# Kernel tuning notes

Hardware: AMD Instinct MI355X
Metric: run time of the kernel (lower is better)

The kernel has to match this reference:

```python
import jax, jax.numpy as jnp
import numpy as np

IN_DIM = 256
QK_DIM = IN_DIM // 8


def setup_inputs() -> dict:
    key = jax.random.key(0)
    ks = jax.random.split(key, 10)
    B, C, W, H = 4, IN_DIM, 64, 64
    a = jax.random.normal(ks[0], (B, C, W, H), dtype=jnp.float32)
    b = jax.random.normal(ks[1], (B, C, W, H), dtype=jnp.float32)
    c = jax.random.uniform(ks[2], (B, 1, 2 * W, 2 * H), dtype=jnp.float32)
    scale = 0.02
    wq = jax.random.normal(ks[3], (QK_DIM, C), dtype=jnp.float32) * scale
    bq = jnp.zeros((QK_DIM,), dtype=jnp.float32)
    wk = jax.random.normal(ks[4], (QK_DIM, C), dtype=jnp.float32) * scale
    bk = jnp.zeros((QK_DIM,), dtype=jnp.float32)
    wv = jax.random.normal(ks[5], (C, C), dtype=jnp.float32) * scale
    bv = jnp.zeros((C,), dtype=jnp.float32)
    gamma = jnp.ones((1,), dtype=jnp.float32)
    return {"a": a, "b": b, "c": c, "wq": wq, "bq": bq, "wk": wk,
            "bk": bk, "wv": wv, "bv": bv, "gamma": gamma}


def reference(a, b, c, wq, bq, wk, bk, wv, bv, gamma):
    B, C, W, H = a.shape
    N = W * H
    # F.interpolate(c, scale_factor=1/down_rate, mode='nearest'): output idx i -> input idx i*down_rate
    down = c.shape[2] // W
    cd = c[:, :, ::down, ::down]                      # [B,1,W,H]
    # 1x1 convs as channel contractions
    q = jnp.einsum('bchw,oc->bohw', a, wq) + bq[None, :, None, None]
    k = jnp.einsum('bchw,oc->bohw', b, wk) + bk[None, :, None, None]
    v = jnp.einsum('bchw,oc->bohw', a, wv) + bv[None, :, None, None]
    qf = q.reshape(B, QK_DIM, N)                      # proj_query^T rows are spatial
    kf = k.reshape(B, QK_DIM, N)
    vf = v.reshape(B, C, N)
    sim = jnp.einsum('bdi,bdj->bij', qf, kf)          # [B,N,N]
    cflat = cd.reshape(B, N)
    # mask[b,i,j] = cflat[b,i] (per-query multiplicative logit scaling)
    logits = sim * cflat[:, :, None]
    attn = jax.nn.softmax(logits, axis=-1)            # [B,N,N]
    out_attn = jnp.einsum('bcj,bij->bci', vf, attn).reshape(B, C, W, H)
    out = gamma * a * cd + (1.0 - cd) * out_attn
    return out
```

## Files before the change

kernel.cpp:

```cpp
#include <hip/hip_runtime.h>

#define LOG2E 1.44269504088896340736f

typedef __attribute__((ext_vector_type(8))) short short8;
typedef __attribute__((ext_vector_type(4))) float float4v;
typedef __attribute__((ext_vector_type(2))) float float2v;
typedef __attribute__((ext_vector_type(2))) int int2v;
typedef __attribute__((ext_vector_type(4))) int int4v;

__device__ inline unsigned short f2bf(float f) {
    union { float f; unsigned u; } v; v.f = f;
    unsigned r = v.u + 0x7fffu + ((v.u >> 16) & 1u);
    return (unsigned short)(r >> 16);
}
__device__ inline float bf2f(unsigned short u) {
    union { unsigned u; float f; } v; v.u = ((unsigned)u) << 16;
    return v.f;
}
__device__ inline unsigned pk_bf16(float a, float b) {
    union { float f; unsigned u; } ua, ub; ua.f = a; ub.f = b;
    return __builtin_amdgcn_perm(ub.u + 0x8000u, ua.u + 0x8000u, 0x07060302u);
}
__device__ inline unsigned cvtpk_bf16(float a, float b) {
    unsigned r;
    asm("v_cvt_pk_bf16_f32 %0, %1, %2" : "=v"(r) : "v"(a), "v"(b));
    return r;
}

__global__ void wcvt_kernel(const float* __restrict__ wq, const float* __restrict__ wk,
                            const float* __restrict__ wv, unsigned short* __restrict__ Wbf)
{
    int idx = blockIdx.x * 256 + threadIdx.x;
    int e4  = idx * 4;
    int row = e4 >> 8, col = e4 & 255;
    const float* src = (row < 32) ? (wq + row * 256 + col)
                     : (row < 64) ? (wk + (row - 32) * 256 + col)
                                  : (wv + (row - 64) * 256 + col);
    float4v v = *(const float4v*)src;
    int2v p;
    p.x = (unsigned)f2bf(v[0]) | ((unsigned)f2bf(v[1]) << 16);
    p.y = (unsigned)f2bf(v[2]) | ((unsigned)f2bf(v[3]) << 16);
    *(int2v*)(Wbf + e4) = p;
}

__launch_bounds__(512, 2)
__global__ void proj_kernel(const float* __restrict__ a_p, const float* __restrict__ b_p,
                            const float* __restrict__ c_p,
                            const float* __restrict__ bq, const float* __restrict__ bk,
                            const float* __restrict__ bv,
                            const unsigned short* __restrict__ Wbf,
                            unsigned short* __restrict__ Qg, unsigned short* __restrict__ Kg,
                            unsigned short* __restrict__ Vg)
{
    __shared__ __align__(16) unsigned short At[64 * 266];
    __shared__ __align__(16) unsigned short Bt[64 * 266];
    __shared__ float bias[320];
    __shared__ float cdl[64];

    const int t    = threadIdx.x;
    const int blk  = blockIdx.x;
    const int b    = blk & 3;
    const int tile = blk >> 2;
    const int i0   = tile * 64;
    const int lane = t & 63;
    const int w    = t >> 6;
    const int q    = lane >> 4;
    const int n    = lane & 15;
    const int it   = w & 3;
    const int mh   = w >> 2;

    {
        const int arr = t >> 8, tt = t & 255;
        unsigned* dst = (unsigned*)(arr ? Bt : At);
        const float* base = (arr ? b_p : a_p) + (size_t)b * 256 * 4096 + i0;
#pragma unroll
        for (int r = 0; r < 8; ++r) {
            int task = r * 256 + tt;
            int cp = task >> 4, px4 = (task & 15) * 4;
            const float* s0 = base + (size_t)(2 * cp) * 4096 + px4;
            float4v r0 = *(const float4v*)s0;
            float4v r1 = *(const float4v*)(s0 + 4096);
#pragma unroll
            for (int k = 0; k < 4; ++k)
                dst[(px4 + k) * 133 + cp] = pk_bf16(r0[k], r1[k]);
        }
        if (t < 320) bias[t] = (t < 32) ? bq[t] : (t < 64) ? bk[t - 32] : bv[t - 64];
        else if (t < 384) cdl[t - 320] = c_p[b * 16384 + tile * 256 + (t - 320) * 2];
    }
    __syncthreads();

    float4v acc[10];
#pragma unroll
    for (int j = 0; j < 10; ++j) acc[j] = (float4v){0.f, 0.f, 0.f, 0.f};

#pragma unroll 2
    for (int kc = 0; kc < 8; ++kc) {
        short8 xa = *(const short8*)&At[(it * 16 + n) * 266 + kc * 32 + q * 8];
        short8 xb = xa;
        if (mh == 0)
            xb = *(const short8*)&Bt[(it * 16 + n) * 266 + kc * 32 + q * 8];
#pragma unroll
        for (int j = 0; j < 10; ++j) {
            int mt = mh * 10 + j;
            short8 wf = *(const short8*)(Wbf + (size_t)(mt * 16 + n) * 256 + kc * 32 + q * 8);
            short8 bsel = (mt == 2 || mt == 3) ? xb : xa;
            acc[j] = __builtin_amdgcn_mfma_f32_16x16x32_bf16(wf, bsel, acc[j], 0, 0, 0);
        }
    }
    __syncthreads();

    unsigned short* QKst = At;
    unsigned short* Vst  = Bt;
    {
        const float cdq = cdl[it * 16 + n] * LOG2E;
#pragma unroll
        for (int j = 0; j < 10; ++j) {
            int mt = mh * 10 + j;
            float4v bv4 = *(const float4v*)&bias[mt * 16 + q * 4];
            float v0 = acc[j][0] + bv4[0], v1 = acc[j][1] + bv4[1];
            float v2 = acc[j][2] + bv4[2], v3 = acc[j][3] + bv4[3];
            if (mt < 2) {
                v0 *= cdq; v1 *= cdq; v2 *= cdq; v3 *= cdq;
                int2v pk; pk.x = (int)pk_bf16(v0, v1); pk.y = (int)pk_bf16(v2, v3);
                *(int2v*)&QKst[(it * 16 + n) * 72 + mt * 16 + q * 4] = pk;
            } else if (mt < 4) {
                int2v pk; pk.x = (int)pk_bf16(v0, v1); pk.y = (int)pk_bf16(v2, v3);
                *(int2v*)&QKst[(it * 16 + n) * 72 + mt * 16 + q * 4] = pk;
            } else {
                int p = ((n >> 2) * 8) + ((it & 1) * 4) + (n & 3);
                int cbase = mt * 16 - 64 + q * 4;
                int jb = it >> 1;
                Vst[((jb * 256) + cbase + 0) * 32 + p] = f2bf(v0);
                Vst[((jb * 256) + cbase + 1) * 32 + p] = f2bf(v1);
                Vst[((jb * 256) + cbase + 2) * 32 + p] = f2bf(v2);
                Vst[((jb * 256) + cbase + 3) * 32 + p] = f2bf(v3);
            }
        }
    }
    __syncthreads();

    {
        int i = t >> 3, h8 = t & 7;
        int4v v = *(const int4v*)&QKst[i * 72 + h8 * 8];
        unsigned short* dstp = (h8 < 4)
            ? Qg + (size_t)(b * 4096 + i0 + i) * 32 + h8 * 8
            : Kg + (size_t)(b * 4096 + i0 + i) * 32 + (h8 - 4) * 8;
        *(int4v*)dstp = v;
    }
    {
#pragma unroll
        for (int k = 0; k < 4; ++k) {
            int flat = k * 512 + t;
            int4v v = *(const int4v*)&Vst[flat * 8];
            int jb = flat >> 10;
            *(int4v*)(Vg + (size_t)(b * 128 + tile * 2 + jb) * 8192 + (flat & 1023) * 8) = v;
        }
    }
}

__launch_bounds__(256, 3)
__global__ void attn_kernel(const unsigned short* __restrict__ Qg,
                            const unsigned short* __restrict__ Kg,
                            const unsigned short* __restrict__ Vg,
                            unsigned short* __restrict__ Opart, float* __restrict__ lsum)
{
    const int t    = threadIdx.x;
    const int blk  = blockIdx.x;
    const int b    = blk & 3;
    const int s_lo = (blk >> 2) & 1;
    const int rt   = (blk >> 3) & 63;
    const int s    = s_lo + 2 * (blk >> 9);
    const int lidx = (s << 8) | (rt << 2) | b;
    const int i0   = rt * 64;
    const int lane = t & 63;
    const int w    = t >> 6;
    const int q    = lane >> 4;
    const int n    = lane & 15;

    union { short8 s8; unsigned u[4]; } ones_;
    ones_.u[0] = ones_.u[1] = ones_.u[2] = ones_.u[3] = 0x3F803F80u;
    const short8 ones8 = ones_.s8;

    short8 qf[4];
#pragma unroll
    for (int ig = 0; ig < 4; ++ig)
        qf[ig] = *(const short8*)(Qg + (size_t)(b * 4096 + i0 + ig * 16 + n) * 32 + q * 8);

    float4v acc[4][4];
    float4v lacc[4];
#pragma unroll
    for (int ig = 0; ig < 4; ++ig) {
        lacc[ig] = (float4v){0.f, 0.f, 0.f, 0.f};
#pragma unroll
        for (int ct = 0; ct < 4; ++ct) acc[ig][ct] = (float4v){0.f, 0.f, 0.f, 0.f};
    }

    const float4v m16v = (float4v){-16.f, -16.f, -16.f, -16.f};

    const unsigned short* kb = Kg + (size_t)(b * 4096 + s * 1024 + n) * 32 + q * 8;
    const unsigned short* vb = Vg + ((size_t)((b * 128 + s * 32) * 256 + w * 64 + n)) * 32 + q * 8;

    short8 kf0 = *(const short8*)(kb);
    short8 kf1 = *(const short8*)(kb + 512);

#pragma unroll 1
    for (int it = 0; it < 32; ++it) {
        short8 vf[4];
#pragma unroll
        for (int ct = 0; ct < 4; ++ct)
            vf[ct] = *(const short8*)(vb + ct * 512);

        short8 pf[4];
#pragma unroll
        for (int ig = 0; ig < 4; ++ig) {
            float4v s0 = __builtin_amdgcn_mfma_f32_16x16x32_bf16(kf0, qf[ig], m16v, 0, 0, 0);
            float4v s1 = __builtin_amdgcn_mfma_f32_16x16x32_bf16(kf1, qf[ig], m16v, 0, 0, 0);
            float p0 = __builtin_amdgcn_exp2f(s0[0]), p1 = __builtin_amdgcn_exp2f(s0[1]);
            float p2 = __builtin_amdgcn_exp2f(s0[2]), p3 = __builtin_amdgcn_exp2f(s0[3]);
            float p4 = __builtin_amdgcn_exp2f(s1[0]), p5 = __builtin_amdgcn_exp2f(s1[1]);
            float p6 = __builtin_amdgcn_exp2f(s1[2]), p7 = __builtin_amdgcn_exp2f(s1[3]);
            union { short8 s8; unsigned u[4]; } pf_;
            pf_.u[0] = cvtpk_bf16(p0, p1);
            pf_.u[1] = cvtpk_bf16(p2, p3);
            pf_.u[2] = cvtpk_bf16(p4, p5);
            pf_.u[3] = cvtpk_bf16(p6, p7);
            pf[ig] = pf_.s8;
        }

        kf0 = *(const short8*)(kb + 1024);
        kf1 = *(const short8*)(kb + 1536);

        __builtin_amdgcn_s_setprio(1);
#pragma unroll
        for (int ig = 0; ig < 4; ++ig) {
            lacc[ig] = __builtin_amdgcn_mfma_f32_16x16x32_bf16(pf[ig], ones8, lacc[ig], 0, 0, 0);
#pragma unroll
            for (int ct = 0; ct < 4; ++ct)
                acc[ig][ct] = __builtin_amdgcn_mfma_f32_16x16x32_bf16(pf[ig], vf[ct], acc[ig][ct], 0, 0, 0);
        }
        __builtin_amdgcn_s_setprio(0);

        kb += 1024;
        vb += 8192;
    }

    const size_t obase = (size_t)lidx * 16384;
#pragma unroll
    for (int ig = 0; ig < 4; ++ig)
#pragma unroll
        for (int ct = 0; ct < 4; ++ct) {
            int c = w * 64 + ct * 16 + n;
            int i = ig * 16 + q * 4;
            int2v pk;
            pk.x = (int)pk_bf16(acc[ig][ct][0], acc[ig][ct][1]);
            pk.y = (int)pk_bf16(acc[ig][ct][2], acc[ig][ct][3]);
            *(int2v*)(Opart + obase + (size_t)c * 64 + i) = pk;
        }
    if (w == 0 && n == 0) {
#pragma unroll
        for (int ig = 0; ig < 4; ++ig)
#pragma unroll
            for (int r = 0; r < 4; ++r)
                lsum[(size_t)lidx * 64 + ig * 16 + q * 4 + r] = lacc[ig][r];
    }
}

__launch_bounds__(256, 4)
__global__ void combine_kernel(const float* __restrict__ a_p, const float* __restrict__ c_p,
                               const float* __restrict__ gamma_p,
                               const unsigned short* __restrict__ Opart,
                               const float* __restrict__ lsum, float* __restrict__ out)
{
    __shared__ float invL[64];
    __shared__ float cdl[64];

    const int t   = threadIdx.x;
    const int blk = blockIdx.x;
    const int b   = blk & 3;
    const int rt  = (blk >> 2) & 63;
    const int cs  = blk >> 8;
    const int i0  = rt * 64;

    if (t < 64) {
        float L = 0.f;
#pragma unroll
        for (int s = 0; s < 4; ++s)
            L += lsum[(size_t)((s << 8) | (rt << 2) | b) * 64 + t];
        invL[t] = 1.0f / L;
        cdl[t] = c_p[b * 16384 + rt * 256 + 2 * t];
    }
    __syncthreads();

    const float gam = gamma_p[0];
    const int il = (t & 31) * 2;
    const int cq = t >> 5;
#pragma unroll
    for (int k = 0; k < 4; ++k) {
        int c = cs * 32 + cq + 8 * k;
        float o0 = 0.f, o1 = 0.f;
#pragma unroll
        for (int s = 0; s < 4; ++s) {
            int idx = (s << 8) | (rt << 2) | b;
            unsigned pr = *(const unsigned*)(Opart + (size_t)idx * 16384 + (size_t)c * 64 + il);
            o0 += bf2f((unsigned short)(pr & 0xffff));
            o1 += bf2f((unsigned short)(pr >> 16));
        }
        o0 *= invL[il];
        o1 *= invL[il + 1];
        size_t gi = (size_t)(b * 256 + c) * 4096 + i0 + il;
        float2v av = *(const float2v*)(a_p + gi);
        float cd0 = cdl[il], cd1 = cdl[il + 1];
        float2v ov;
        ov[0] = gam * av[0] * cd0 + (1.0f - cd0) * o0;
        ov[1] = gam * av[1] * cd1 + (1.0f - cd1) * o1;
        *(float2v*)(out + gi) = ov;
    }
}

extern "C" void kernel_launch(void* const* d_in, const int* in_sizes, int n_in,
                              void* d_out, int out_size, void* d_ws, size_t ws_size,
                              hipStream_t stream)
{
    const float* a_p   = (const float*)d_in[0];
    const float* b_p   = (const float*)d_in[1];
    const float* c_p   = (const float*)d_in[2];
    const float* wq    = (const float*)d_in[3];
    const float* bq    = (const float*)d_in[4];
    const float* wk    = (const float*)d_in[5];
    const float* bk    = (const float*)d_in[6];
    const float* wv    = (const float*)d_in[7];
    const float* bv    = (const float*)d_in[8];
    const float* gamma = (const float*)d_in[9];
    float* out = (float*)d_out;

    unsigned short* Qg    = (unsigned short*)d_ws;
    unsigned short* Kg    = Qg + (size_t)4 * 4096 * 32;
    unsigned short* Vg    = Kg + (size_t)4 * 4096 * 32;
    unsigned short* Wbf   = Vg + (size_t)4 * 256 * 4096;
    unsigned short* Opart = Wbf + (size_t)320 * 256;
    float*          lsum  = (float*)(Opart + (size_t)1024 * 16384);

    wcvt_kernel<<<80, 256, 0, stream>>>(wq, wk, wv, Wbf);
    proj_kernel<<<256, 512, 0, stream>>>(a_p, b_p, c_p, bq, bk, bv, Wbf, Qg, Kg, Vg);
    attn_kernel<<<1024, 256, 0, stream>>>(Qg, Kg, Vg, Opart, lsum);
    combine_kernel<<<2048, 256, 0, stream>>>(a_p, c_p, gamma, Opart, lsum, out);
}
```

Before: 182.2 us.

## Software-pipeline attention loop and compute row sums with VALU instead of MFMA

The attention loop is restructured into a one-stage software pipeline. Each iteration issues the QK MFMAs for the next key tile while the PV MFMAs for the previous tile run, and the exp2/convert work is placed after the V loads so it can overlap them. The row-sum MFMA against a ones vector is dropped. Row sums are instead accumulated in fp32 VALU adds over the unrounded probabilities and reduced across lanes with shuffles at the end. This removes one MFMA per ig per iteration but adds VALU adds and register pressure for the extra in-flight score and probability registers, and the sums are now taken before the bf16 rounding applied to the probabilities.

```diff
diff --git a/kernel.cpp b/kernel.cpp
--- a/kernel.cpp
+++ b/kernel.cpp
@@ -177,72 +177,105 @@
     const int q    = lane >> 4;
     const int n    = lane & 15;
 
-    union { short8 s8; unsigned u[4]; } ones_;
-    ones_.u[0] = ones_.u[1] = ones_.u[2] = ones_.u[3] = 0x3F803F80u;
-    const short8 ones8 = ones_.s8;
-
     short8 qf[4];
 #pragma unroll
     for (int ig = 0; ig < 4; ++ig)
         qf[ig] = *(const short8*)(Qg + (size_t)(b * 4096 + i0 + ig * 16 + n) * 32 + q * 8);
 
     float4v acc[4][4];
-    float4v lacc[4];
-#pragma unroll
-    for (int ig = 0; ig < 4; ++ig) {
-        lacc[ig] = (float4v){0.f, 0.f, 0.f, 0.f};
+#pragma unroll
+    for (int ig = 0; ig < 4; ++ig)
 #pragma unroll
         for (int ct = 0; ct < 4; ++ct) acc[ig][ct] = (float4v){0.f, 0.f, 0.f, 0.f};
-    }
+    float lsc[4] = {0.f, 0.f, 0.f, 0.f};
 
     const float4v m16v = (float4v){-16.f, -16.f, -16.f, -16.f};
 
     const unsigned short* kb = Kg + (size_t)(b * 4096 + s * 1024 + n) * 32 + q * 8;
     const unsigned short* vb = Vg + ((size_t)((b * 128 + s * 32) * 256 + w * 64 + n)) * 32 + q * 8;
 
+    short8 vf[4];
+#pragma unroll
+    for (int ct = 0; ct < 4; ++ct)
+        vf[ct] = *(const short8*)(vb + ct * 512);
     short8 kf0 = *(const short8*)(kb);
     short8 kf1 = *(const short8*)(kb + 512);
 
-#pragma unroll 1
-    for (int it = 0; it < 32; ++it) {
-        short8 vf[4];
-#pragma unroll
-        for (int ct = 0; ct < 4; ++ct)
-            vf[ct] = *(const short8*)(vb + ct * 512);
-
-        short8 pf[4];
+    short8 pfc[4];
+    {
+        float4v s0[4], s1[4];
 #pragma unroll
         for (int ig = 0; ig < 4; ++ig) {
-            float4v s0 = __builtin_amdgcn_mfma_f32_16x16x32_bf16(kf0, qf[ig], m16v, 0, 0, 0);
-            float4v s1 = __builtin_amdgcn_mfma_f32_16x16x32_bf16(kf1, qf[ig], m16v, 0, 0, 0);
-            float p0 = __builtin_amdgcn_exp2f(s0[0]), p1 = __builtin_amdgcn_exp2f(s0[1]);
-            float p2 = __builtin_amdgcn_exp2f(s0[2]), p3 = __builtin_amdgcn_exp2f(s0[3]);
-            float p4 = __builtin_amdgcn_exp2f(s1[0]), p5 = __builtin_amdgcn_exp2f(s1[1]);
-            float p6 = __builtin_amdgcn_exp2f(s1[2]), p7 = __builtin_amdgcn_exp2f(s1[3]);
+            s0[ig] = __builtin_amdgcn_mfma_f32_16x16x32_bf16(kf0, qf[ig], m16v, 0, 0, 0);
+            s1[ig] = __builtin_amdgcn_mfma_f32_16x16x32_bf16(kf1, qf[ig], m16v, 0, 0, 0);
+        }
+        kf0 = *(const short8*)(kb + 1024);
+        kf1 = *(const short8*)(kb + 1536);
+#pragma unroll
+        for (int ig = 0; ig < 4; ++ig) {
+            float p0 = __builtin_amdgcn_exp2f(s0[ig][0]), p1 = __builtin_amdgcn_exp2f(s0[ig][1]);
+            float p2 = __builtin_amdgcn_exp2f(s0[ig][2]), p3 = __builtin_amdgcn_exp2f(s0[ig][3]);
+            float p4 = __builtin_amdgcn_exp2f(s1[ig][0]), p5 = __builtin_amdgcn_exp2f(s1[ig][1]);
+            float p6 = __builtin_amdgcn_exp2f(s1[ig][2]), p7 = __builtin_amdgcn_exp2f(s1[ig][3]);
+            lsc[ig] += ((p0 + p1) + (p2 + p3)) + ((p4 + p5) + (p6 + p7));
             union { short8 s8; unsigned u[4]; } pf_;
             pf_.u[0] = cvtpk_bf16(p0, p1);
             pf_.u[1] = cvtpk_bf16(p2, p3);
             pf_.u[2] = cvtpk_bf16(p4, p5);
             pf_.u[3] = cvtpk_bf16(p6, p7);
-            pf[ig] = pf_.s8;
-        }
-
-        kf0 = *(const short8*)(kb + 1024);
-        kf1 = *(const short8*)(kb + 1536);
+            pfc[ig] = pf_.s8;
+        }
+    }
+    kb += 2048;
+    vb += 8192;
+
+#pragma unroll 1
+    for (int it = 0; it < 31; ++it) {
+        float4v s0[4], s1[4];
+#pragma unroll
+        for (int ig = 0; ig < 4; ++ig) {
+            s0[ig] = __builtin_amdgcn_mfma_f32_16x16x32_bf16(kf0, qf[ig], m16v, 0, 0, 0);
+            s1[ig] = __builtin_amdgcn_mfma_f32_16x16x32_bf16(kf1, qf[ig], m16v, 0, 0, 0);
+        }
+        kf0 = *(const short8*)(kb);
+        kf1 = *(const short8*)(kb + 512);
 
         __builtin_amdgcn_s_setprio(1);
 #pragma unroll
+        for (int ig = 0; ig < 4; ++ig)
+#pragma unroll
+            for (int ct = 0; ct < 4; ++ct)
+                acc[ig][ct] = __builtin_amdgcn_mfma_f32_16x16x32_bf16(pfc[ig], vf[ct], acc[ig][ct], 0, 0, 0);
+        __builtin_amdgcn_s_setprio(0);
+
+#pragma unroll
+        for (int ct = 0; ct < 4; ++ct)
+            vf[ct] = *(const short8*)(vb + ct * 512);
+
+#pragma unroll
         for (int ig = 0; ig < 4; ++ig) {
-            lacc[ig] = __builtin_amdgcn_mfma_f32_16x16x32_bf16(pf[ig], ones8, lacc[ig], 0, 0, 0);
-#pragma unroll
-            for (int ct = 0; ct < 4; ++ct)
-                acc[ig][ct] = __builtin_amdgcn_mfma_f32_16x16x32_bf16(pf[ig], vf[ct], acc[ig][ct], 0, 0, 0);
-        }
-        __builtin_amdgcn_s_setprio(0);
+            float p0 = __builtin_amdgcn_exp2f(s0[ig][0]), p1 = __builtin_amdgcn_exp2f(s0[ig][1]);
+            float p2 = __builtin_amdgcn_exp2f(s0[ig][2]), p3 = __builtin_amdgcn_exp2f(s0[ig][3]);
+            float p4 = __builtin_amdgcn_exp2f(s1[ig][0]), p5 = __builtin_amdgcn_exp2f(s1[ig][1]);
+            float p6 = __builtin_amdgcn_exp2f(s1[ig][2]), p7 = __builtin_amdgcn_exp2f(s1[ig][3]);
+            lsc[ig] += ((p0 + p1) + (p2 + p3)) + ((p4 + p5) + (p6 + p7));
+            union { short8 s8; unsigned u[4]; } pf_;
+            pf_.u[0] = cvtpk_bf16(p0, p1);
+            pf_.u[1] = cvtpk_bf16(p2, p3);
+            pf_.u[2] = cvtpk_bf16(p4, p5);
+            pf_.u[3] = cvtpk_bf16(p6, p7);
+            pfc[ig] = pf_.s8;
+        }
 
         kb += 1024;
         vb += 8192;
     }
+
+#pragma unroll
+    for (int ig = 0; ig < 4; ++ig)
+#pragma unroll
+        for (int ct = 0; ct < 4; ++ct)
+            acc[ig][ct] = __builtin_amdgcn_mfma_f32_16x16x32_bf16(pfc[ig], vf[ct], acc[ig][ct], 0, 0, 0);
 
     const size_t obase = (size_t)lidx * 16384;
 #pragma unroll
@@ -256,12 +289,13 @@
             pk.y = (int)pk_bf16(acc[ig][ct][2], acc[ig][ct][3]);
             *(int2v*)(Opart + obase + (size_t)c * 64 + i) = pk;
         }
-    if (w == 0 && n == 0) {
-#pragma unroll
-        for (int ig = 0; ig < 4; ++ig)
-#pragma unroll
-            for (int r = 0; r < 4; ++r)
-                lsum[(size_t)lidx * 64 + ig * 16 + q * 4 + r] = lacc[ig][r];
+#pragma unroll
+    for (int ig = 0; ig < 4; ++ig) {
+        float v = lsc[ig];
+        v += __shfl_xor(v, 16, 64);
+        v += __shfl_xor(v, 32, 64);
+        if (w == 0 && lane < 16)
+            lsum[(size_t)lidx * 64 + ig * 16 + lane] = v;
     }
 }
 
```

Result: no change. 183.1 us (+0.5%).
